# Kernel optimization log

Measured on AMD Instinct MI355X. Metric: run time of the kernel, lower is better.

Reference implementation:

```python
import jax, jax.numpy as jnp
import numpy as np

DIM = 768
NUM_HEADS = 12
HEAD_DIM = DIM // NUM_HEADS
SCALE = HEAD_DIM ** -0.5
KEEP_NUM = 160


def setup_inputs() -> dict:
    key = jax.random.key(0)
    k0, k1, k2, k3 = jax.random.split(key, 4)
    B, N, C = 64, 197, DIM
    x = jax.random.normal(k0, (B, N, C), dtype=jnp.float32)
    # torch nn.Linear weights: [out_features, in_features]
    qkv_w = jax.random.normal(k1, (3 * C, C), dtype=jnp.float32) * (C ** -0.5)
    proj_w = jax.random.normal(k2, (C, C), dtype=jnp.float32) * (C ** -0.5)
    proj_b = jax.random.normal(k3, (C,), dtype=jnp.float32) * 0.01
    return {"x": x, "qkv_w": qkv_w, "proj_w": proj_w, "proj_b": proj_b}


def reference(x, qkv_w, proj_w, proj_b):
    B, N, C = x.shape
    H, D = NUM_HEADS, HEAD_DIM
    # qkv: [B, N, 3, H, D] -> q,k,v each [B, H, N, D]
    qkv = (x @ qkv_w.T).reshape(B, N, 3, H, D)
    qkv = jnp.transpose(qkv, (2, 0, 3, 1, 4))
    q, k, v = qkv[0], qkv[1], qkv[2]
    # raw pre-softmax scores [B, H, N, N]
    attn = jnp.einsum('bhnd,bhmd->bhnm', q, k) * SCALE
    # SUM_ABS_1: CLS row of scores, abs-summed over heads -> [B, N]
    attn_weight = jnp.sum(jnp.abs(attn[:, :, 0, :]), axis=1)
    # top_pool: keep top KEEP_NUM tokens by weight, indices sorted ascending
    _, idx = jax.lax.top_k(attn_weight, KEEP_NUM)
    keep_index = jnp.sort(idx, axis=-1)
    # standard attention
    attn = jax.nn.softmax(attn, axis=-1)
    out = jnp.einsum('bhnm,bhmd->bhnd', attn, v)
    out = jnp.transpose(out, (0, 2, 1, 3)).reshape(B, N, C)
    out = out @ proj_w.T + proj_b
    return out, keep_index
```

## Files before the change

kernel.cpp:

```cpp
#include <hip/hip_runtime.h>
#include <hip/hip_bf16.h>


#define BB 64
#define NN 197
#define CC 768
#define HH 12
#define DD 64
#define KEEP 160
#define SCALE_F 0.125f
#define OUT0_ELEMS ((size_t)BB * NN * CC)
#define VST 212

typedef __attribute__((ext_vector_type(8))) short bf16x8_t;
typedef __attribute__((ext_vector_type(4))) float f32x4_t;

__device__ __forceinline__ float b2f(unsigned short u) {
  union { unsigned u; float f; } cv; cv.u = (unsigned)u << 16; return cv.f;
}
__device__ __forceinline__ unsigned short f2b(float f) {
  union { float f; unsigned u; } cv; cv.f = f;
  return (unsigned short)((cv.u + 0x7FFFu + ((cv.u >> 16) & 1u)) >> 16);
}
__device__ __forceinline__ float ldmix(const void* p, size_t i, int f32) {
  return f32 ? ((const float*)p)[i] : b2f(((const unsigned short*)p)[i]);
}
__device__ __forceinline__ bf16x8_t ld8(const unsigned short* p) {
  short4 a = *(const short4*)p;
  short4 b = *(const short4*)(p + 4);
  bf16x8_t v = {a.x, a.y, a.z, a.w, b.x, b.y, b.z, b.w};
  return v;
}
__device__ __forceinline__ void gload16(const unsigned short* g,
                                        unsigned short* s) {
  __builtin_amdgcn_global_load_lds(
      (const __attribute__((address_space(1))) void*)g,
      (__attribute__((address_space(3))) void*)s, 16, 0, 0);
}

__global__ void detect_kernel(const void* x, int* flag) {
  __shared__ int cnt;
  if (threadIdx.x == 0) cnt = 0;
  __syncthreads();
  const unsigned short* u = (const unsigned short*)x;
  int wild = 0;
  for (int i = threadIdx.x; i < 4096; i += 256) {
    int e = (u[i] >> 7) & 0xFF;
    wild += (e >= 140);
  }
  atomicAdd(&cnt, wild);
  __syncthreads();
  if (threadIdx.x == 0) *flag = (cnt > 100) ? 1 : 0;
}

__global__ void cvt_all(const void* qkv_w, const void* proj_w, const void* proj_b,
                        unsigned short* wb, unsigned short* pw, float* pbf,
                        const int* flag) {
  const int W3 = 3 * CC * CC, W1 = CC * CC;
  int i = blockIdx.x * 256 + threadIdx.x;
  const int f32 = *flag;
  if (i < W3) {
    wb[i] = f32 ? f2b(((const float*)qkv_w)[i]) : ((const unsigned short*)qkv_w)[i];
  } else if (i < W3 + W1) {
    int j = i - W3;
    pw[j] = f32 ? f2b(((const float*)proj_w)[j]) : ((const unsigned short*)proj_w)[j];
  } else if (i < W3 + W1 + CC) {
    int j = i - W3 - W1;
    pbf[j] = ldmix(proj_b, j, f32);
  }
}

__global__ void cvt_x(const void* __restrict__ x, size_t elem_off,
                      unsigned short* __restrict__ xb, int n8,
                      const int* __restrict__ flag) {
  const int i = blockIdx.x * 256 + threadIdx.x;
  if (i >= n8) return;
  const size_t src = elem_off + (size_t)i * 8;
  bf16x8_t v;
  if (*flag) {
    const float* xp = (const float*)x + src;
    float4 u0 = *(const float4*)xp;
    float4 u1 = *(const float4*)(xp + 4);
    v = bf16x8_t{(short)f2b(u0.x), (short)f2b(u0.y), (short)f2b(u0.z),
                 (short)f2b(u0.w), (short)f2b(u1.x), (short)f2b(u1.y),
                 (short)f2b(u1.z), (short)f2b(u1.w)};
  } else {
    v = *(const bf16x8_t*)((const unsigned short*)x + src);
  }
  *(bf16x8_t*)(xb + (size_t)i * 8) = v;
}

__global__ __launch_bounds__(256, 4) void qkv_gemm(
    const unsigned short* __restrict__ xb,
    const unsigned short* __restrict__ wb,
    unsigned short* __restrict__ qkvc, int Mc, int bc, int nRow) {
  const int xcd = blockIdx.x & 7;
  const int seq = blockIdx.x >> 3;
  const int colt = seq % 18;
  const int rowt = (seq / 18) * 8 + xcd;
  if (rowt >= nRow) return;
  const int m0 = rowt * 128;
  const int n0 = colt * 128;

  __shared__ unsigned short lds[16640];
  const int lane = threadIdx.x & 63;
  const int wave = threadIdx.x >> 6;
  const int l16  = lane & 15;
  const int quad = lane >> 4;
  const int wm = wave >> 1, wn = wave & 1;

  const int rS   = wave * 16 + (lane >> 2);
  const int koff = (lane & 3) * 8;
  int grA0 = m0 + rS;       if (grA0 >= Mc) grA0 = Mc - 1;
  int grA1 = m0 + rS + 64;  if (grA1 >= Mc) grA1 = Mc - 1;
  const unsigned short* gA0 = xb + (size_t)grA0 * CC + koff;
  const unsigned short* gA1 = xb + (size_t)grA1 * CC + koff;
  const unsigned short* gB0 = wb + (size_t)(n0 + rS) * CC + koff;
  const unsigned short* gB1 = wb + (size_t)(n0 + rS + 64) * CC + koff;
  unsigned short* const sA0 = lds + wave * 512;
  unsigned short* const sA1 = lds + 2048 + wave * 512;
  unsigned short* const sB0 = lds + 8192 + wave * 512;
  unsigned short* const sB1 = lds + 8192 + 2048 + wave * 512;

  gload16(gA0, sA0); gload16(gA1, sA1);
  gload16(gB0, sB0); gload16(gB1, sB1);
  gA0 += 32; gA1 += 32; gB0 += 32; gB1 += 32;

  f32x4_t acc[4][4] = {};
  #pragma unroll 2
  for (int kt = 0; kt < 24; kt++) {
    const int ro = (kt & 1) << 12;
    const int so = ro ^ 4096;
    if (kt < 23) {
      gload16(gA0, sA0 + so); gload16(gA1, sA1 + so);
      gload16(gB0, sB0 + so); gload16(gB1, sB1 + so);
      gA0 += 32; gA1 += 32; gB0 += 32; gB1 += 32;
      asm volatile("s_waitcnt vmcnt(4)" ::: "memory");
    } else {
      asm volatile("s_waitcnt vmcnt(0)" ::: "memory");
    }
    __builtin_amdgcn_s_barrier();
    bf16x8_t afr[4], bfr[4];
    #pragma unroll
    for (int r = 0; r < 4; r++)
      afr[r] = *(const bf16x8_t*)&lds[ro + (wm * 4 + r) * 512 + l16 * 32 + quad * 8];
    #pragma unroll
    for (int c = 0; c < 4; c++)
      bfr[c] = *(const bf16x8_t*)&lds[8192 + ro + (wn * 4 + c) * 512 + l16 * 32 + quad * 8];
    asm volatile("s_waitcnt lgkmcnt(0)" ::: "memory");
    __builtin_amdgcn_s_barrier();
    #pragma unroll
    for (int r = 0; r < 4; r++)
      #pragma unroll
      for (int c = 0; c < 4; c++)
        acc[r][c] = __builtin_amdgcn_mfma_f32_16x16x32_bf16(afr[r], bfr[c],
                                                            acc[r][c], 0, 0, 0);
  }

  #pragma unroll
  for (int c = 0; c < 4; c++)
    #pragma unroll
    for (int r = 0; r < 4; r++)
      #pragma unroll
      for (int i = 0; i < 4; i++)
        lds[(wm * 64 + r * 16 + quad * 4 + i) * 130 + wn * 64 + c * 16 + l16] =
            f2b(acc[r][c][i]);
  __syncthreads();
  {
    const int row = threadIdx.x >> 1;
    const int seg = threadIdx.x & 1;
    const int m = m0 + row;
    if (m < Mc) {
      const int col0 = n0 + seg * 64;
      const int s = col0 / CC;
      const int rem = col0 - s * CC;
      const int hc = rem >> 6;
      const int bb2 = m / NN, n = m - bb2 * NN;
      unsigned short* dst =
          qkvc + ((((size_t)s * bc + bb2) * HH + hc) * NN + n) * DD;
      const unsigned short* srcr = lds + row * 130 + seg * 64;
      #pragma unroll
      for (int j = 0; j < 8; j++) {
        uint4 v;
        v.x = *(const unsigned*)(srcr + j * 8 + 0);
        v.y = *(const unsigned*)(srcr + j * 8 + 2);
        v.z = *(const unsigned*)(srcr + j * 8 + 4);
        v.w = *(const unsigned*)(srcr + j * 8 + 6);
        *(uint4*)(dst + j * 8) = v;
      }
    }
  }
}

__global__ __launch_bounds__(256, 4) void proj_gemm(
    const unsigned short* __restrict__ Yc,
    const unsigned short* __restrict__ pw,
    const float* __restrict__ pbf,
    void* __restrict__ out, size_t out_off, int Mc, int nRow,
    const int* __restrict__ flag) {
  const int xcd = blockIdx.x & 7;
  const int seq = blockIdx.x >> 3;
  const int colt = seq % 6;
  const int rowt = (seq / 6) * 8 + xcd;
  if (rowt >= nRow) return;
  const int m0 = rowt * 128;
  const int n0 = colt * 128;

  __shared__ unsigned short lds[17152];
  const int lane = threadIdx.x & 63;
  const int wave = threadIdx.x >> 6;
  const int l16  = lane & 15;
  const int quad = lane >> 4;
  const int wm = wave >> 1, wn = wave & 1;

  const int rS   = wave * 16 + (lane >> 2);
  const int koff = (lane & 3) * 8;
  int grA0 = m0 + rS;       if (grA0 >= Mc) grA0 = Mc - 1;
  int grA1 = m0 + rS + 64;  if (grA1 >= Mc) grA1 = Mc - 1;
  const unsigned short* gA0 = Yc + (size_t)grA0 * CC + koff;
  const unsigned short* gA1 = Yc + (size_t)grA1 * CC + koff;
  const unsigned short* gB0 = pw + (size_t)(n0 + rS) * CC + koff;
  const unsigned short* gB1 = pw + (size_t)(n0 + rS + 64) * CC + koff;
  unsigned short* const sA0 = lds + wave * 512;
  unsigned short* const sA1 = lds + 2048 + wave * 512;
  unsigned short* const sB0 = lds + 8192 + wave * 512;
  unsigned short* const sB1 = lds + 8192 + 2048 + wave * 512;

  gload16(gA0, sA0); gload16(gA1, sA1);
  gload16(gB0, sB0); gload16(gB1, sB1);
  gA0 += 32; gA1 += 32; gB0 += 32; gB1 += 32;

  f32x4_t acc[4][4] = {};
  #pragma unroll 2
  for (int kt = 0; kt < 24; kt++) {
    const int ro = (kt & 1) << 12;
    const int so = ro ^ 4096;
    if (kt < 23) {
      gload16(gA0, sA0 + so); gload16(gA1, sA1 + so);
      gload16(gB0, sB0 + so); gload16(gB1, sB1 + so);
      gA0 += 32; gA1 += 32; gB0 += 32; gB1 += 32;
      asm volatile("s_waitcnt vmcnt(4)" ::: "memory");
    } else {
      asm volatile("s_waitcnt vmcnt(0)" ::: "memory");
    }
    __builtin_amdgcn_s_barrier();
    bf16x8_t afr[4], bfr[4];
    #pragma unroll
    for (int r = 0; r < 4; r++)
      afr[r] = *(const bf16x8_t*)&lds[ro + (wm * 4 + r) * 512 + l16 * 32 + quad * 8];
    #pragma unroll
    for (int c = 0; c < 4; c++)
      bfr[c] = *(const bf16x8_t*)&lds[8192 + ro + (wn * 4 + c) * 512 + l16 * 32 + quad * 8];
    asm volatile("s_waitcnt lgkmcnt(0)" ::: "memory");
    __builtin_amdgcn_s_barrier();
    #pragma unroll
    for (int r = 0; r < 4; r++)
      #pragma unroll
      for (int c = 0; c < 4; c++)
        acc[r][c] = __builtin_amdgcn_mfma_f32_16x16x32_bf16(afr[r], bfr[c],
                                                            acc[r][c], 0, 0, 0);
  }

  const int f32o = *flag;
  float* Cf = (float*)lds;
  #pragma unroll
  for (int p = 0; p < 2; p++) {
    __syncthreads();
    if (wn == p) {
      #pragma unroll
      for (int c = 0; c < 4; c++) {
        const float bv = pbf[n0 + wn * 64 + c * 16 + l16];
        #pragma unroll
        for (int r = 0; r < 4; r++)
          #pragma unroll
          for (int i = 0; i < 4; i++)
            Cf[(wm * 64 + r * 16 + quad * 4 + i) * 67 + c * 16 + l16] =
                acc[r][c][i] + bv;
      }
    }
    __syncthreads();
    const int row = threadIdx.x >> 1;
    const int part = threadIdx.x & 1;
    const int m = m0 + row;
    if (m < Mc) {
      const float* srcr = Cf + row * 67 + part * 32;
      const size_t ob = out_off + (size_t)m * CC + n0 + p * 64 + part * 32;
      if (f32o) {
        float* dst = (float*)out + ob;
        #pragma unroll
        for (int j = 0; j < 8; j++) {
          float4 v = {srcr[j * 4], srcr[j * 4 + 1], srcr[j * 4 + 2],
                      srcr[j * 4 + 3]};
          *(float4*)(dst + j * 4) = v;
        }
      } else {
        unsigned short* dst = (unsigned short*)out + ob;
        #pragma unroll
        for (int j = 0; j < 4; j++) {
          uint4 v;
          v.x = (unsigned)f2b(srcr[j * 8 + 0]) | ((unsigned)f2b(srcr[j * 8 + 1]) << 16);
          v.y = (unsigned)f2b(srcr[j * 8 + 2]) | ((unsigned)f2b(srcr[j * 8 + 3]) << 16);
          v.z = (unsigned)f2b(srcr[j * 8 + 4]) | ((unsigned)f2b(srcr[j * 8 + 5]) << 16);
          v.w = (unsigned)f2b(srcr[j * 8 + 6]) | ((unsigned)f2b(srcr[j * 8 + 7]) << 16);
          *(uint4*)(dst + j * 8) = v;
        }
      }
    }
  }
}

__global__ __launch_bounds__(256, 3) void attn_kernel(
    const unsigned short* __restrict__ qkvc, int bc,
    unsigned short* __restrict__ Yc) {
  const int bh = blockIdx.x;
  const int bb = bh / HH;
  const int h  = bh % HH;
  const size_t mat = (size_t)bc * HH * NN * DD;
  const unsigned short* q = qkvc + ((size_t)bb * HH + h) * NN * DD;
  const unsigned short* k = q + mat;
  const unsigned short* v = q + 2 * mat;

  __shared__ unsigned short Vt[DD * VST];
  __shared__ unsigned short Pl[4][16 * VST];

  const int lane = threadIdx.x & 63;
  const int wave = threadIdx.x >> 6;
  const int l16  = lane & 15;
  const int quad = lane >> 4;

  #pragma unroll
  for (int it = 0; it < 53; it++) {
    const int key = it * 4 + wave;
    unsigned short val = (key < NN) ? v[(size_t)key * DD + lane]
                                    : (unsigned short)0;
    Vt[lane * VST + key] = val;
  }
  __syncthreads();

  unsigned short* Pw = &Pl[wave][0];

  for (int it = 0; it < 4; it++) {
    const int si = it * 4 + wave;
    if (si >= 13) break;
    const int q0 = si * 16;

    int qrow = q0 + l16; if (qrow >= NN) qrow = NN - 1;
    const unsigned short* qp = q + (size_t)qrow * DD + quad * 8;
    const bf16x8_t aq0 = *(const bf16x8_t*)qp;
    const bf16x8_t aq1 = *(const bf16x8_t*)(qp + 32);

    f32x4_t sc[13];
    #pragma unroll
    for (int ct = 0; ct < 13; ct++) {
      int key = ct * 16 + l16; if (key >= NN) key = NN - 1;
      const unsigned short* kp = k + (size_t)key * DD + quad * 8;
      const bf16x8_t b0 = *(const bf16x8_t*)kp;
      const bf16x8_t b1 = *(const bf16x8_t*)(kp + 32);
      f32x4_t t = {0.f, 0.f, 0.f, 0.f};
      t = __builtin_amdgcn_mfma_f32_16x16x32_bf16(aq0, b0, t, 0, 0, 0);
      t = __builtin_amdgcn_mfma_f32_16x16x32_bf16(aq1, b1, t, 0, 0, 0);
      sc[ct] = t;
    }

    float inv_l[4];
    #pragma unroll
    for (int i = 0; i < 4; i++) {
      float m = -1e30f;
      #pragma unroll
      for (int ct = 0; ct < 13; ct++)
        if (ct < 12 || l16 < 5) m = fmaxf(m, sc[ct][i] * SCALE_F);
      #pragma unroll
      for (int d = 1; d < 16; d <<= 1) m = fmaxf(m, __shfl_xor(m, d, 64));
      float s = 0.f;
      #pragma unroll
      for (int ct = 0; ct < 13; ct++) {
        const float p = (ct < 12 || l16 < 5) ? __expf(sc[ct][i] * SCALE_F - m)
                                             : 0.f;
        sc[ct][i] = p;
        s += p;
      }
      #pragma unroll
      for (int d = 1; d < 16; d <<= 1) s += __shfl_xor(s, d, 64);
      inv_l[i] = 1.0f / s;
    }

    #pragma unroll
    for (int i = 0; i < 4; i++) {
      const int ro = (quad * 4 + i) * VST;
      #pragma unroll
      for (int ct = 0; ct < 13; ct++)
        Pw[ro + ct * 16 + l16] = f2b(sc[ct][i]);
    }

    f32x4_t oc[4] = {};
    #pragma unroll
    for (int ks = 0; ks < 6; ks++) {
      const bf16x8_t ap = ld8(&Pw[l16 * VST + ks * 32 + quad * 8]);
      #pragma unroll
      for (int dt = 0; dt < 4; dt++) {
        const bf16x8_t bv = ld8(&Vt[(dt * 16 + l16) * VST + ks * 32 + quad * 8]);
        oc[dt] = __builtin_amdgcn_mfma_f32_16x16x32_bf16(ap, bv, oc[dt], 0, 0, 0);
      }
    }
    {
      const bf16x8_t zz = {};
      bf16x8_t ap = zz;
      if (quad < 2) ap = ld8(&Pw[l16 * VST + 192 + quad * 8]);
      #pragma unroll
      for (int dt = 0; dt < 4; dt++) {
        bf16x8_t bv = zz;
        if (quad < 2) bv = ld8(&Vt[(dt * 16 + l16) * VST + 192 + quad * 8]);
        oc[dt] = __builtin_amdgcn_mfma_f32_16x16x32_bf16(ap, bv, oc[dt], 0, 0, 0);
      }
    }

    #pragma unroll
    for (int i = 0; i < 4; i++) {
      const int n = q0 + quad * 4 + i;
      if (n < NN) {
        unsigned short* yp = Yc + ((size_t)bb * NN + n) * CC + h * DD;
        #pragma unroll
        for (int dt = 0; dt < 4; dt++)
          yp[dt * 16 + l16] = f2b(oc[dt][i] * inv_l[i]);
      }
    }
  }
}

__global__ __launch_bounds__(256, 4) void qcls_kernel(
    const void* __restrict__ x, const void* __restrict__ qkv_w,
    float* __restrict__ qc, const int* __restrict__ flag) {
  const int idx = blockIdx.x * 4 + (threadIdx.x >> 6);
  if (idx >= BB * CC) return;
  const int b = idx / CC, i = idx - b * CC;
  const int lane = threadIdx.x & 63;
  const int f32 = *flag;
  const size_t xr = (size_t)b * NN * CC;
  const size_t wr = (size_t)i * CC;
  float p = 0.f;
  #pragma unroll
  for (int j = 0; j < 12; j++)
    p += ldmix(x, xr + j * 64 + lane, f32) * ldmix(qkv_w, wr + j * 64 + lane, f32);
  #pragma unroll
  for (int m = 32; m; m >>= 1) p += __shfl_xor(p, m, 64);
  if (lane == 0) qc[(size_t)b * CC + i] = p;
}

__global__ __launch_bounds__(256, 2) void gmat_kernel(
    const void* __restrict__ qkv_w, const float* __restrict__ qc,
    float* __restrict__ g, const int* __restrict__ flag) {
  const int h = blockIdx.x, c0 = blockIdx.y * 128;
  const int f32 = *flag;
  __shared__ float Wt[64][128];
  __shared__ float qh[64][64];
  for (int t = threadIdx.x; t < 64 * 128; t += 256) {
    const int d = t >> 7, c = t & 127;
    Wt[d][c] = ldmix(qkv_w, (size_t)(CC + h * DD + d) * CC + c0 + c, f32);
  }
  for (int t = threadIdx.x; t < 64 * 64; t += 256) {
    const int b = t >> 6, d = t & 63;
    qh[b][d] = qc[(size_t)b * CC + h * DD + d];
  }
  __syncthreads();
  const int c = threadIdx.x & 127;
  const int bg = (threadIdx.x >> 7) * 32;
  for (int bi = 0; bi < 32; bi++) {
    const int b = bg + bi;
    float a = 0.f;
    #pragma unroll
    for (int d = 0; d < 64; d++) a += qh[b][d] * Wt[d][c];
    g[((size_t)b * HH + h) * CC + c0 + c] = a;
  }
}

__global__ __launch_bounds__(256, 4) void score_kernel(
    const void* __restrict__ x, const float* __restrict__ g,
    float* __restrict__ wscore, const int* __restrict__ flag) {
  const int idx = blockIdx.x * 4 + (threadIdx.x >> 6);
  if (idx >= BB * NN) return;
  const int b = idx / NN, n = idx - b * NN;
  const int lane = threadIdx.x & 63;
  const int f32 = *flag;
  const size_t xr = ((size_t)b * NN + n) * CC;
  float xv[12];
  #pragma unroll
  for (int j = 0; j < 12; j++) xv[j] = ldmix(x, xr + j * 64 + lane, f32);
  const float* gb = g + (size_t)b * HH * CC;
  float acc = 0.f;
  #pragma unroll
  for (int h = 0; h < HH; h++) {
    const float* gh = gb + (size_t)h * CC;
    float p = 0.f;
    #pragma unroll
    for (int j = 0; j < 12; j++) p += xv[j] * gh[j * 64 + lane];
    #pragma unroll
    for (int m = 32; m; m >>= 1) p += __shfl_xor(p, m, 64);
    acc += fabsf(p);
  }
  if (lane == 0) wscore[(size_t)b * NN + n] = acc;
}

__global__ __launch_bounds__(256, 4) void rank_kernel(
    const float* __restrict__ wscore, void* __restrict__ out,
    const int* __restrict__ flag) {
  const int b = blockIdx.x;
  const int f32 = *flag;
  __shared__ float wgt[NN];
  __shared__ int   rank[NN];
  if (threadIdx.x < NN) wgt[threadIdx.x] = wscore[(size_t)b * NN + threadIdx.x];
  __syncthreads();
  const int n = threadIdx.x;
  if (n < NN) {
    float wi = wgt[n];
    int rk = 0;
    for (int j = 0; j < NN; j++) {
      float wj = wgt[j];
      rk += (wj > wi) || (wj == wi && j < n);
    }
    rank[n] = rk;
  }
  __syncthreads();
  if (n < NN && rank[n] < KEEP) {
    int pos = 0;
    for (int j = 0; j < n; j++) pos += (rank[j] < KEEP);
    const size_t oi = OUT0_ELEMS + (size_t)b * KEEP + pos;
    if (f32) ((float*)out)[oi] = (float)n;
    else ((unsigned short*)out)[oi] = f2b((float)n);
  }
}

extern "C" void kernel_launch(void* const* d_in, const int* in_sizes, int n_in,
                              void* d_out, int out_size, void* d_ws, size_t ws_size,
                              hipStream_t stream) {
  const void* x      = d_in[0];
  const void* qkv_w  = d_in[1];
  const void* proj_w = d_in[2];
  const void* proj_b = d_in[3];

  char* wsb = (char*)d_ws;
  int* flag = (int*)wsb;
  unsigned short* wb  = (unsigned short*)(wsb + 256);
  unsigned short* pw  = (unsigned short*)(wsb + 256 + 3538944);
  float* pbf    = (float*)(wsb + 256 + 3538944 + 1179648);
  float* qc     = (float*)(wsb + 256 + 3538944 + 1179648 + 4096);
  float* g      = qc + (size_t)BB * CC;
  float* wscore = g + (size_t)BB * HH * CC;
  const size_t fixed = 256 + 3538944 + 1179648 + 4096 + 196608 + 2359296 + 51200;
  char* chunk = wsb + fixed;

  const size_t per_batch = (size_t)NN * CC * 2
                         + 3ull * HH * NN * DD * 2
                         + (size_t)NN * CC * 2;
  int Bc = BB;
  while (Bc > 1 && fixed + (size_t)Bc * per_batch > ws_size) Bc >>= 1;

  unsigned short* xb   = (unsigned short*)chunk;
  unsigned short* qkvc = xb + (size_t)Bc * NN * CC;
  unsigned short* Yc   = qkvc + 3ull * Bc * HH * NN * DD;

  detect_kernel<<<1, 256, 0, stream>>>(x, flag);
  const int cvt_n = 3 * CC * CC + CC * CC + CC;
  cvt_all<<<(cvt_n + 255) / 256, 256, 0, stream>>>(qkv_w, proj_w, proj_b,
                                                   wb, pw, pbf, flag);

  qcls_kernel<<<(BB * CC + 3) / 4, 256, 0, stream>>>(x, qkv_w, qc, flag);
  gmat_kernel<<<dim3(HH, 6), 256, 0, stream>>>(qkv_w, qc, g, flag);
  score_kernel<<<(BB * NN + 3) / 4, 256, 0, stream>>>(x, g, wscore, flag);
  rank_kernel<<<BB, 256, 0, stream>>>(wscore, d_out, flag);

  const int nChunks = (BB + Bc - 1) / Bc;
  for (int cb = 0; cb < nChunks; cb++) {
    const int b0 = cb * Bc;
    const int bc = (BB - b0 < Bc) ? (BB - b0) : Bc;
    const int Mc = bc * NN;
    const int n8 = Mc * CC / 8;
    cvt_x<<<(n8 + 255) / 256, 256, 0, stream>>>(
        x, (size_t)b0 * NN * CC, xb, n8, flag);
    const int nRowQ = (Mc + 127) / 128;
    const int gridQ = 8 * 18 * ((nRowQ + 7) / 8);
    qkv_gemm<<<gridQ, 256, 0, stream>>>(xb, wb, qkvc, Mc, bc, nRowQ);
    attn_kernel<<<dim3(bc * HH), 256, 0, stream>>>(qkvc, bc, Yc);
    const int gridP = 8 * 6 * ((nRowQ + 7) / 8);
    proj_gemm<<<gridP, 256, 0, stream>>>(
        Yc, pw, pbf, d_out, (size_t)b0 * NN * CC, Mc, nRowQ, flag);
  }
}
```

Before: 383.9 us.

## Replace double-buffered K pipeline with single-buffer K=64 steps in GEMMs

Both GEMM kernels (QKV projection and output projection) drop the software-pipelined double buffer with explicit vmcnt waits. They now load a 64-wide K slab (two 32-wide halves) into LDS, synchronise, and run 32 MFMAs per iteration over 12 iterations instead of 24. This halves the number of barrier rounds and simplifies the waitcnt logic. In exchange, global loads no longer overlap with MFMA compute inside a block, so latency hiding falls back on other resident blocks.

Measured after the change: 507.9 us. 32.3% more time.

```diff
diff --git a/kernel.cpp b/kernel.cpp
--- a/kernel.cpp
+++ b/kernel.cpp
@@ -117,45 +117,44 @@
   const unsigned short* gA1 = xb + (size_t)grA1 * CC + koff;
   const unsigned short* gB0 = wb + (size_t)(n0 + rS) * CC + koff;
   const unsigned short* gB1 = wb + (size_t)(n0 + rS + 64) * CC + koff;
-  unsigned short* const sA0 = lds + wave * 512;
-  unsigned short* const sA1 = lds + 2048 + wave * 512;
-  unsigned short* const sB0 = lds + 8192 + wave * 512;
-  unsigned short* const sB1 = lds + 8192 + 2048 + wave * 512;
-
-  gload16(gA0, sA0); gload16(gA1, sA1);
-  gload16(gB0, sB0); gload16(gB1, sB1);
-  gA0 += 32; gA1 += 32; gB0 += 32; gB1 += 32;
+  unsigned short* const dA = lds + wave * 512;
+  unsigned short* const dB = lds + 8192 + wave * 512;
 
   f32x4_t acc[4][4] = {};
-  #pragma unroll 2
-  for (int kt = 0; kt < 24; kt++) {
-    const int ro = (kt & 1) << 12;
-    const int so = ro ^ 4096;
-    if (kt < 23) {
-      gload16(gA0, sA0 + so); gload16(gA1, sA1 + so);
-      gload16(gB0, sB0 + so); gload16(gB1, sB1 + so);
-      gA0 += 32; gA1 += 32; gB0 += 32; gB1 += 32;
-      asm volatile("s_waitcnt vmcnt(4)" ::: "memory");
-    } else {
-      asm volatile("s_waitcnt vmcnt(0)" ::: "memory");
-    }
-    __builtin_amdgcn_s_barrier();
-    bf16x8_t afr[4], bfr[4];
-    #pragma unroll
-    for (int r = 0; r < 4; r++)
-      afr[r] = *(const bf16x8_t*)&lds[ro + (wm * 4 + r) * 512 + l16 * 32 + quad * 8];
-    #pragma unroll
-    for (int c = 0; c < 4; c++)
-      bfr[c] = *(const bf16x8_t*)&lds[8192 + ro + (wn * 4 + c) * 512 + l16 * 32 + quad * 8];
-    asm volatile("s_waitcnt lgkmcnt(0)" ::: "memory");
-    __builtin_amdgcn_s_barrier();
-    #pragma unroll
-    for (int r = 0; r < 4; r++)
+  for (int kt = 0; kt < 12; kt++) {
+    __syncthreads();
+    gload16(gA0,      dA);
+    gload16(gA1,      dA + 2048);
+    gload16(gA0 + 32, dA + 4096);
+    gload16(gA1 + 32, dA + 6144);
+    gload16(gB0,      dB);
+    gload16(gB1,      dB + 2048);
+    gload16(gB0 + 32, dB + 4096);
+    gload16(gB1 + 32, dB + 6144);
+    gA0 += 64; gA1 += 64; gB0 += 64; gB1 += 64;
+    __syncthreads();
+    bf16x8_t afr[2][4], bfr[2][4];
+    #pragma unroll
+    for (int kk = 0; kk < 2; kk++) {
+      #pragma unroll
+      for (int r = 0; r < 4; r++)
+        afr[kk][r] = *(const bf16x8_t*)
+            &lds[kk * 4096 + (wm * 4 + r) * 512 + l16 * 32 + quad * 8];
       #pragma unroll
       for (int c = 0; c < 4; c++)
-        acc[r][c] = __builtin_amdgcn_mfma_f32_16x16x32_bf16(afr[r], bfr[c],
-                                                            acc[r][c], 0, 0, 0);
-  }
+        bfr[kk][c] = *(const bf16x8_t*)
+            &lds[8192 + kk * 4096 + (wn * 4 + c) * 512 + l16 * 32 + quad * 8];
+    }
+    #pragma unroll
+    for (int kk = 0; kk < 2; kk++)
+      #pragma unroll
+      for (int r = 0; r < 4; r++)
+        #pragma unroll
+        for (int c = 0; c < 4; c++)
+          acc[r][c] = __builtin_amdgcn_mfma_f32_16x16x32_bf16(
+              afr[kk][r], bfr[kk][c], acc[r][c], 0, 0, 0);
+  }
+  __syncthreads();
 
   #pragma unroll
   for (int c = 0; c < 4; c++)
@@ -221,45 +220,44 @@
   const unsigned short* gA1 = Yc + (size_t)grA1 * CC + koff;
   const unsigned short* gB0 = pw + (size_t)(n0 + rS) * CC + koff;
   const unsigned short* gB1 = pw + (size_t)(n0 + rS + 64) * CC + koff;
-  unsigned short* const sA0 = lds + wave * 512;
-  unsigned short* const sA1 = lds + 2048 + wave * 512;
-  unsigned short* const sB0 = lds + 8192 + wave * 512;
-  unsigned short* const sB1 = lds + 8192 + 2048 + wave * 512;
-
-  gload16(gA0, sA0); gload16(gA1, sA1);
-  gload16(gB0, sB0); gload16(gB1, sB1);
-  gA0 += 32; gA1 += 32; gB0 += 32; gB1 += 32;
+  unsigned short* const dA = lds + wave * 512;
+  unsigned short* const dB = lds + 8192 + wave * 512;
 
   f32x4_t acc[4][4] = {};
-  #pragma unroll 2
-  for (int kt = 0; kt < 24; kt++) {
-    const int ro = (kt & 1) << 12;
-    const int so = ro ^ 4096;
-    if (kt < 23) {
-      gload16(gA0, sA0 + so); gload16(gA1, sA1 + so);
-      gload16(gB0, sB0 + so); gload16(gB1, sB1 + so);
-      gA0 += 32; gA1 += 32; gB0 += 32; gB1 += 32;
-      asm volatile("s_waitcnt vmcnt(4)" ::: "memory");
-    } else {
-      asm volatile("s_waitcnt vmcnt(0)" ::: "memory");
-    }
-    __builtin_amdgcn_s_barrier();
-    bf16x8_t afr[4], bfr[4];
-    #pragma unroll
-    for (int r = 0; r < 4; r++)
-      afr[r] = *(const bf16x8_t*)&lds[ro + (wm * 4 + r) * 512 + l16 * 32 + quad * 8];
-    #pragma unroll
-    for (int c = 0; c < 4; c++)
-      bfr[c] = *(const bf16x8_t*)&lds[8192 + ro + (wn * 4 + c) * 512 + l16 * 32 + quad * 8];
-    asm volatile("s_waitcnt lgkmcnt(0)" ::: "memory");
-    __builtin_amdgcn_s_barrier();
-    #pragma unroll
-    for (int r = 0; r < 4; r++)
+  for (int kt = 0; kt < 12; kt++) {
+    __syncthreads();
+    gload16(gA0,      dA);
+    gload16(gA1,      dA + 2048);
+    gload16(gA0 + 32, dA + 4096);
+    gload16(gA1 + 32, dA + 6144);
+    gload16(gB0,      dB);
+    gload16(gB1,      dB + 2048);
+    gload16(gB0 + 32, dB + 4096);
+    gload16(gB1 + 32, dB + 6144);
+    gA0 += 64; gA1 += 64; gB0 += 64; gB1 += 64;
+    __syncthreads();
+    bf16x8_t afr[2][4], bfr[2][4];
+    #pragma unroll
+    for (int kk = 0; kk < 2; kk++) {
+      #pragma unroll
+      for (int r = 0; r < 4; r++)
+        afr[kk][r] = *(const bf16x8_t*)
+            &lds[kk * 4096 + (wm * 4 + r) * 512 + l16 * 32 + quad * 8];
       #pragma unroll
       for (int c = 0; c < 4; c++)
-        acc[r][c] = __builtin_amdgcn_mfma_f32_16x16x32_bf16(afr[r], bfr[c],
-                                                            acc[r][c], 0, 0, 0);
-  }
+        bfr[kk][c] = *(const bf16x8_t*)
+            &lds[8192 + kk * 4096 + (wn * 4 + c) * 512 + l16 * 32 + quad * 8];
+    }
+    #pragma unroll
+    for (int kk = 0; kk < 2; kk++)
+      #pragma unroll
+      for (int r = 0; r < 4; r++)
+        #pragma unroll
+        for (int c = 0; c < 4; c++)
+          acc[r][c] = __builtin_amdgcn_mfma_f32_16x16x32_bf16(
+              afr[kk][r], bfr[kk][c], acc[r][c], 0, 0, 0);
+  }
+  __syncthreads();
 
   const int f32o = *flag;
   float* Cf = (float*)lds;
```

## Swizzle GEMM LDS k-chunks and re-grid gmat kernel per batch-head

Applied to the files above, without the earlier changes.

Applies an XOR swizzle to the k-chunk offset used when staging A/B tiles into LDS in the QKV and projection GEMMs, with the matching swizzle on the MFMA fragment reads, to reduce LDS bank conflicts. It also rewrites gmat_kernel from a 72-block shared-memory tile scheme into a 768-block grid (one block per batch and head) that streams the key-weight rows directly. The gmat change gives more parallelism but re-reads the same weight rows for every batch, leaning on L2.

Measured after the change: 374.3 us (median of 3 runs). -2.5%, faster.

```diff
diff --git a/kernel.cpp b/kernel.cpp
--- a/kernel.cpp
+++ b/kernel.cpp
@@ -110,7 +110,7 @@
   const int wm = wave >> 1, wn = wave & 1;
 
   const int rS   = wave * 16 + (lane >> 2);
-  const int koff = (lane & 3) * 8;
+  const int koff = ((lane & 3) ^ ((lane >> 3) & 3)) * 8;
   int grA0 = m0 + rS;       if (grA0 >= Mc) grA0 = Mc - 1;
   int grA1 = m0 + rS + 64;  if (grA1 >= Mc) grA1 = Mc - 1;
   const unsigned short* gA0 = xb + (size_t)grA0 * CC + koff;
@@ -121,6 +121,8 @@
   unsigned short* const sA1 = lds + 2048 + wave * 512;
   unsigned short* const sB0 = lds + 8192 + wave * 512;
   unsigned short* const sB1 = lds + 8192 + 2048 + wave * 512;
+
+  const int kgs = (quad ^ ((l16 >> 1) & 3)) * 8;
 
   gload16(gA0, sA0); gload16(gA1, sA1);
   gload16(gB0, sB0); gload16(gB1, sB1);
@@ -143,10 +145,10 @@
     bf16x8_t afr[4], bfr[4];
     #pragma unroll
     for (int r = 0; r < 4; r++)
-      afr[r] = *(const bf16x8_t*)&lds[ro + (wm * 4 + r) * 512 + l16 * 32 + quad * 8];
+      afr[r] = *(const bf16x8_t*)&lds[ro + (wm * 4 + r) * 512 + l16 * 32 + kgs];
     #pragma unroll
     for (int c = 0; c < 4; c++)
-      bfr[c] = *(const bf16x8_t*)&lds[8192 + ro + (wn * 4 + c) * 512 + l16 * 32 + quad * 8];
+      bfr[c] = *(const bf16x8_t*)&lds[8192 + ro + (wn * 4 + c) * 512 + l16 * 32 + kgs];
     asm volatile("s_waitcnt lgkmcnt(0)" ::: "memory");
     __builtin_amdgcn_s_barrier();
     #pragma unroll
@@ -214,7 +216,7 @@
   const int wm = wave >> 1, wn = wave & 1;
 
   const int rS   = wave * 16 + (lane >> 2);
-  const int koff = (lane & 3) * 8;
+  const int koff = ((lane & 3) ^ ((lane >> 3) & 3)) * 8;
   int grA0 = m0 + rS;       if (grA0 >= Mc) grA0 = Mc - 1;
   int grA1 = m0 + rS + 64;  if (grA1 >= Mc) grA1 = Mc - 1;
   const unsigned short* gA0 = Yc + (size_t)grA0 * CC + koff;
@@ -225,6 +227,8 @@
   unsigned short* const sA1 = lds + 2048 + wave * 512;
   unsigned short* const sB0 = lds + 8192 + wave * 512;
   unsigned short* const sB1 = lds + 8192 + 2048 + wave * 512;
+
+  const int kgs = (quad ^ ((l16 >> 1) & 3)) * 8;
 
   gload16(gA0, sA0); gload16(gA1, sA1);
   gload16(gB0, sB0); gload16(gB1, sB1);
@@ -247,10 +251,10 @@
     bf16x8_t afr[4], bfr[4];
     #pragma unroll
     for (int r = 0; r < 4; r++)
-      afr[r] = *(const bf16x8_t*)&lds[ro + (wm * 4 + r) * 512 + l16 * 32 + quad * 8];
+      afr[r] = *(const bf16x8_t*)&lds[ro + (wm * 4 + r) * 512 + l16 * 32 + kgs];
     #pragma unroll
     for (int c = 0; c < 4; c++)
-      bfr[c] = *(const bf16x8_t*)&lds[8192 + ro + (wn * 4 + c) * 512 + l16 * 32 + quad * 8];
+      bfr[c] = *(const bf16x8_t*)&lds[8192 + ro + (wn * 4 + c) * 512 + l16 * 32 + kgs];
     asm volatile("s_waitcnt lgkmcnt(0)" ::: "memory");
     __builtin_amdgcn_s_barrier();
     #pragma unroll
@@ -446,31 +450,25 @@
   if (lane == 0) qc[(size_t)b * CC + i] = p;
 }
 
-__global__ __launch_bounds__(256, 2) void gmat_kernel(
+__global__ __launch_bounds__(256, 4) void gmat_kernel(
     const void* __restrict__ qkv_w, const float* __restrict__ qc,
     float* __restrict__ g, const int* __restrict__ flag) {
-  const int h = blockIdx.x, c0 = blockIdx.y * 128;
+  const int b = blockIdx.x, h = blockIdx.y;
   const int f32 = *flag;
-  __shared__ float Wt[64][128];
-  __shared__ float qh[64][64];
-  for (int t = threadIdx.x; t < 64 * 128; t += 256) {
-    const int d = t >> 7, c = t & 127;
-    Wt[d][c] = ldmix(qkv_w, (size_t)(CC + h * DD + d) * CC + c0 + c, f32);
-  }
-  for (int t = threadIdx.x; t < 64 * 64; t += 256) {
-    const int b = t >> 6, d = t & 63;
-    qh[b][d] = qc[(size_t)b * CC + h * DD + d];
-  }
-  __syncthreads();
-  const int c = threadIdx.x & 127;
-  const int bg = (threadIdx.x >> 7) * 32;
-  for (int bi = 0; bi < 32; bi++) {
-    const int b = bg + bi;
-    float a = 0.f;
-    #pragma unroll
-    for (int d = 0; d < 64; d++) a += qh[b][d] * Wt[d][c];
-    g[((size_t)b * HH + h) * CC + c0 + c] = a;
-  }
+  __shared__ float qh[DD];
+  if (threadIdx.x < DD) qh[threadIdx.x] = qc[(size_t)b * CC + h * DD + threadIdx.x];
+  __syncthreads();
+  const int c0 = threadIdx.x, c1 = c0 + 256, c2 = c1 + 256;
+  float a0 = 0.f, a1 = 0.f, a2 = 0.f;
+  for (int d = 0; d < DD; d++) {
+    const size_t ro = (size_t)(CC + h * DD + d) * CC;
+    const float qv = qh[d];
+    a0 += ldmix(qkv_w, ro + c0, f32) * qv;
+    a1 += ldmix(qkv_w, ro + c1, f32) * qv;
+    a2 += ldmix(qkv_w, ro + c2, f32) * qv;
+  }
+  float* gb = g + ((size_t)b * HH + h) * CC;
+  gb[c0] = a0; gb[c1] = a1; gb[c2] = a2;
 }
 
 __global__ __launch_bounds__(256, 4) void score_kernel(
@@ -564,7 +562,7 @@
                                                    wb, pw, pbf, flag);
 
   qcls_kernel<<<(BB * CC + 3) / 4, 256, 0, stream>>>(x, qkv_w, qc, flag);
-  gmat_kernel<<<dim3(HH, 6), 256, 0, stream>>>(qkv_w, qc, g, flag);
+  gmat_kernel<<<dim3(BB, HH), 256, 0, stream>>>(qkv_w, qc, g, flag);
   score_kernel<<<(BB * NN + 3) / 4, 256, 0, stream>>>(x, g, wscore, flag);
   rank_kernel<<<BB, 256, 0, stream>>>(wscore, d_out, flag);
 
```
